# Performance work log

Measured on AMD Instinct MI355X. Metric: run time of the kernel, lower is better.

The kernel has to match this reference:

```python
import jax, jax.numpy as jnp
import numpy as np

D_MODEL = 1024
NUM_HEADS = 16
HEAD_DIM = D_MODEL // NUM_HEADS


def setup_inputs() -> dict:
    key = jax.random.key(0)
    ks = jax.random.split(key, 11)
    B, S = 4, 2048
    s = 1.0 / np.sqrt(D_MODEL)
    inp = {
        "query": jax.random.normal(ks[0], (B, S, D_MODEL), jnp.float32),
        "key": jax.random.normal(ks[1], (B, S, D_MODEL), jnp.float32),
        "value": jax.random.normal(ks[2], (B, S, D_MODEL), jnp.float32),
        "Wq": jax.random.normal(ks[3], (D_MODEL, D_MODEL), jnp.float32) * s,
        "bq": jnp.zeros((D_MODEL,), jnp.float32),
        "Wk": jax.random.normal(ks[4], (D_MODEL, D_MODEL), jnp.float32) * s,
        "bk": jnp.zeros((D_MODEL,), jnp.float32),
        "Wv": jax.random.normal(ks[5], (D_MODEL, D_MODEL), jnp.float32) * s,
        "bv": jnp.zeros((D_MODEL,), jnp.float32),
        "Wo": jax.random.normal(ks[6], (D_MODEL, D_MODEL), jnp.float32) * s,
        "bo": jnp.zeros((D_MODEL,), jnp.float32),
    }
    return inp


def reference(query, key, value, Wq, bq, Wk, bk, Wv, bv, Wo, bo):
    B, S, _ = query.shape
    def proj(x, W, b):  # [B,S,D] -> [B,H,S,hd]
        y = jnp.einsum("bsd,ed->bse", x, W) + b
        return y.reshape(B, -1, NUM_HEADS, HEAD_DIM).transpose(0, 2, 1, 3)
    q = proj(query, Wq, bq)
    k = proj(key, Wk, bk)
    v = proj(value, Wv, bv)
    scores = jnp.einsum("bhqd,bhkd->bhqk", q, k) / np.sqrt(HEAD_DIM).astype(jnp.float32)
    attn = jax.nn.softmax(scores, axis=-1)
    out = jnp.einsum("bhqk,bhkd->bhqd", attn, v)
    out = out.transpose(0, 2, 1, 3).reshape(B, -1, D_MODEL)
    return jnp.einsum("bsd,ed->bse", out, Wo) + bo
```

## Files before the change

### kernel.cpp

```cpp
#include <hip/hip_runtime.h>
#include <math.h>

#define DM    1024
#define NH    16
#define HD    64
#define SEQ   2048
#define BATCH 4
#define TOKENS (BATCH * SEQ)

typedef _Float16 half2v __attribute__((ext_vector_type(2)));
typedef __fp16   fp16x2 __attribute__((ext_vector_type(2)));
typedef _Float16 half4  __attribute__((ext_vector_type(4)));
typedef _Float16 half8  __attribute__((ext_vector_type(8)));
typedef float    f32x4  __attribute__((ext_vector_type(4)));
typedef float    f32x16 __attribute__((ext_vector_type(16)));
typedef unsigned int u32x2 __attribute__((ext_vector_type(2)));
typedef unsigned int u32x4 __attribute__((ext_vector_type(4)));

typedef const __attribute__((address_space(1))) void* gas_p;
typedef __attribute__((address_space(3))) void*       las_p;

__device__ __forceinline__ void gload_lds16(const void* g, void* l) {
    __builtin_amdgcn_global_load_lds((gas_p)g, (las_p)l, 16, 0, 0);
}

__device__ __forceinline__ unsigned pack2u(float a, float b) {
    fp16x2 r = __builtin_amdgcn_cvt_pkrtz(a, b);
    return __builtin_bit_cast(unsigned, r);
}

#define MFMA16(a, b, c) __builtin_amdgcn_mfma_f32_16x16x32_f16((a), (b), (c), 0, 0, 0)
#define MFMA32(a, b, c) __builtin_amdgcn_mfma_f32_32x32x16_f16((a), (b), (c), 0, 0, 0)

__global__ __launch_bounds__(256) void cvt_all(
    const float* __restrict__ q, const float* __restrict__ k,
    const float* __restrict__ v, const float* __restrict__ wq,
    const float* __restrict__ wk, const float* __restrict__ wv,
    const float* __restrict__ wo, _Float16* __restrict__ dst)
{
    const size_t TD = (size_t)TOKENS * DM, WD = (size_t)DM * DM;
    const size_t i = ((size_t)blockIdx.x * 256 + threadIdx.x) * 4;
    const float* s; size_t off;
    if      (i <     TD)          { s = q;  off = i; }
    else if (i < 2 * TD)          { s = k;  off = i - TD; }
    else if (i < 3 * TD)          { s = v;  off = i - 2 * TD; }
    else if (i < 3 * TD + WD)     { s = wq; off = i - 3 * TD; }
    else if (i < 3 * TD + 2 * WD) { s = wk; off = i - 3 * TD - WD; }
    else if (i < 3 * TD + 3 * WD) { s = wv; off = i - 3 * TD - 2 * WD; }
    else                          { s = wo; off = i - 3 * TD - 3 * WD; }
    const float4 x = *(const float4*)(s + off);
    half4 h = { (_Float16)x.x, (_Float16)x.y, (_Float16)x.z, (_Float16)x.w };
    *(half4*)(dst + i) = h;
}

__global__ __launch_bounds__(256) void qkv_gemm(
    const _Float16* __restrict__ Abase, const _Float16* __restrict__ Wbase,
    const float* __restrict__ bq, const float* __restrict__ bk,
    const float* __restrict__ bv, _Float16* __restrict__ Cbase, float qscale)
{
    __shared__ __align__(16) _Float16 As[128 * 32];
    __shared__ __align__(16) _Float16 Ws[128 * 32];

    const int z = blockIdx.z;
    const size_t TD = (size_t)TOKENS * DM, WD = (size_t)DM * DM;
    const _Float16* A = Abase + (size_t)z * TD;
    const _Float16* W = Wbase + (size_t)z * WD;
    const float* bias = (z == 0) ? bq : (z == 1) ? bk : bv;
    _Float16* C = Cbase + (size_t)z * TD;
    const float scale = (z == 0) ? qscale : 1.0f;

    const int t = threadIdx.x;
    const int w = t >> 6, l = t & 63;
    const int tx = l & 15, quad = l >> 4;
    const int m0 = blockIdx.x * 128, n0 = blockIdx.y * 128;
    const int wm = (w & 1) * 64, wn = (w >> 1) * 64;
    const int srow = t >> 2, schk = t & 3;

    const _Float16* Ag = A + (size_t)m0 * DM;
    const _Float16* Wg = W + (size_t)n0 * DM;

    f32x4 acc[4][4] = {};

    for (int k0 = 0; k0 < DM; k0 += 32) {
        __syncthreads();
        #pragma unroll
        for (int i = 0; i < 2; ++i) {
            gload_lds16(Ag + (size_t)(i * 64 + srow) * DM + k0 + schk * 8,
                        As + (size_t)(i * 256 + (t & ~63)) * 8);
            gload_lds16(Wg + (size_t)(i * 64 + srow) * DM + k0 + schk * 8,
                        Ws + (size_t)(i * 256 + (t & ~63)) * 8);
        }
        __syncthreads();

        half8 af[4], bf[4];
        #pragma unroll
        for (int mt = 0; mt < 4; ++mt)
            af[mt] = *(const half8*)(As + (wm + mt * 16 + tx) * 32 + quad * 8);
        #pragma unroll
        for (int nt = 0; nt < 4; ++nt)
            bf[nt] = *(const half8*)(Ws + (wn + nt * 16 + tx) * 32 + quad * 8);
        #pragma unroll
        for (int mt = 0; mt < 4; ++mt)
            #pragma unroll
            for (int nt = 0; nt < 4; ++nt)
                acc[mt][nt] = MFMA16(af[mt], bf[nt], acc[mt][nt]);
    }

    float bsv[4];
    #pragma unroll
    for (int nt = 0; nt < 4; ++nt) bsv[nt] = bias[n0 + wn + nt * 16 + tx];

    #pragma unroll
    for (int mt = 0; mt < 4; ++mt) {
        #pragma unroll
        for (int nt = 0; nt < 4; ++nt) {
            const int n = n0 + wn + nt * 16 + tx;
            const int mr0 = m0 + wm + mt * 16 + quad * 4;
            const int h = n >> 6, d = n & 63;
            if (z < 2) {
                #pragma unroll
                for (int r = 0; r < 4; ++r) {
                    const int m = mr0 + r;
                    const int b = m >> 11, s = m & (SEQ - 1);
                    const float vv = (acc[mt][nt][r] + bsv[nt]) * scale;
                    C[(((size_t)b * NH + h) * SEQ + s) * HD + d] = (_Float16)vv;
                }
            } else {
                const int b = mr0 >> 11, s0 = mr0 & (SEQ - 1);
                half4 hv = { (_Float16)(acc[mt][nt][0] + bsv[nt]),
                             (_Float16)(acc[mt][nt][1] + bsv[nt]),
                             (_Float16)(acc[mt][nt][2] + bsv[nt]),
                             (_Float16)(acc[mt][nt][3] + bsv[nt]) };
                *(half4*)(C + (((size_t)b * NH + h) * HD + d) * SEQ + s0) = hv;
            }
        }
    }
}

__global__ __launch_bounds__(256) void out_gemm(
    const _Float16* __restrict__ A, const _Float16* __restrict__ W,
    const float* __restrict__ bias, float* __restrict__ C)
{
    __shared__ __align__(16) _Float16 As[128 * 32];
    __shared__ __align__(16) _Float16 Ws[128 * 32];

    const int t = threadIdx.x;
    const int w = t >> 6, l = t & 63;
    const int tx = l & 15, quad = l >> 4;
    const int m0 = blockIdx.x * 128, n0 = blockIdx.y * 128;
    const int wm = (w & 1) * 64, wn = (w >> 1) * 64;
    const int srow = t >> 2, schk = t & 3;

    const _Float16* Ag = A + (size_t)m0 * DM;
    const _Float16* Wg = W + (size_t)n0 * DM;

    f32x4 acc[4][4] = {};

    for (int k0 = 0; k0 < DM; k0 += 32) {
        __syncthreads();
        #pragma unroll
        for (int i = 0; i < 2; ++i) {
            gload_lds16(Ag + (size_t)(i * 64 + srow) * DM + k0 + schk * 8,
                        As + (size_t)(i * 256 + (t & ~63)) * 8);
            gload_lds16(Wg + (size_t)(i * 64 + srow) * DM + k0 + schk * 8,
                        Ws + (size_t)(i * 256 + (t & ~63)) * 8);
        }
        __syncthreads();

        half8 af[4], bf[4];
        #pragma unroll
        for (int mt = 0; mt < 4; ++mt)
            af[mt] = *(const half8*)(As + (wm + mt * 16 + tx) * 32 + quad * 8);
        #pragma unroll
        for (int nt = 0; nt < 4; ++nt)
            bf[nt] = *(const half8*)(Ws + (wn + nt * 16 + tx) * 32 + quad * 8);
        #pragma unroll
        for (int mt = 0; mt < 4; ++mt)
            #pragma unroll
            for (int nt = 0; nt < 4; ++nt)
                acc[mt][nt] = MFMA16(af[mt], bf[nt], acc[mt][nt]);
    }

    float bsv[4];
    #pragma unroll
    for (int nt = 0; nt < 4; ++nt) bsv[nt] = bias[n0 + wn + nt * 16 + tx];

    #pragma unroll
    for (int mt = 0; mt < 4; ++mt)
        #pragma unroll
        for (int nt = 0; nt < 4; ++nt) {
            const int n = n0 + wn + nt * 16 + tx;
            const int mr0 = m0 + wm + mt * 16 + quad * 4;
            #pragma unroll
            for (int r = 0; r < 4; ++r)
                C[(size_t)(mr0 + r) * DM + n] = acc[mt][nt][r] + bsv[nt];
        }
}

__global__ __launch_bounds__(256, 3) void flash16(
    const _Float16* __restrict__ Q, const _Float16* __restrict__ K,
    const _Float16* __restrict__ Vt, _Float16* __restrict__ AO)
{
    __shared__ __align__(16) char pool[34816];
    __shared__ float lW[128];

    const int t = threadIdx.x, w = t >> 6, l = t & 63;
    const int lid = l & 31, hl = l >> 5;

    const int bid = blockIdx.x;
    const int xcd = bid & 7, loc = bid >> 3;
    const int bh = xcd * 8 + (loc >> 4);
    const int q0 = (loc & 15) * 128;
    const int b = bh >> 4, h = bh & 15;

    const _Float16* Qg = Q + ((size_t)bh * SEQ + q0 + w * 32) * HD;
    const _Float16* Kg = K + (size_t)bh * SEQ * HD;
    const _Float16* Vg = Vt + (size_t)bh * HD * SEQ;

    const int srow = l >> 3;
    const int schk = (l & 7) ^ srow;

    half8 Qf[4];
    #pragma unroll
    for (int ks = 0; ks < 4; ++ks)
        Qf[ks] = *(const half8*)(Qg + (size_t)lid * HD + ks * 16 + hl * 8);

    f32x16 Oa[2] = {};
    float l2 = 0.f;
    const half2v one2 = { (_Float16)1.0f, (_Float16)1.0f };

    {
        _Float16* KL = (_Float16*)(pool);
        _Float16* VL = (_Float16*)(pool + 16384);
        #pragma unroll
        for (int jj = 0; jj < 2; ++jj) {
            const int j = w + jj * 4;
            const int row = 8 * j + srow;
            gload_lds16(Kg + (size_t)row * HD + schk * 8, KL + j * 512);
            gload_lds16(Vg + (size_t)row * SEQ + schk * 8, VL + j * 512);
        }
    }

    for (int it = 0; it < SEQ / 64; ++it) {
        __syncthreads();

        if (it < SEQ / 64 - 1) {
            const int kb = (it + 1) * 64;
            _Float16* KL = (_Float16*)(pool + ((it + 1) & 1) * 8192);
            _Float16* VL = (_Float16*)(pool + 16384 + ((it + 1) & 1) * 8192);
            #pragma unroll
            for (int jj = 0; jj < 2; ++jj) {
                const int j = w + jj * 4;
                const int row = 8 * j + srow;
                gload_lds16(Kg + (size_t)(kb + row) * HD + schk * 8, KL + j * 512);
                gload_lds16(Vg + (size_t)row * SEQ + kb + schk * 8, VL + j * 512);
            }
        }

        const _Float16* KL = (const _Float16*)(pool + (it & 1) * 8192);
        const _Float16* VL = (const _Float16*)(pool + 16384 + (it & 1) * 8192);

        half8 kf[2][4];
        #pragma unroll
        for (int kt = 0; kt < 2; ++kt)
            #pragma unroll
            for (int ks = 0; ks < 4; ++ks)
                kf[kt][ks] = *(const half8*)(KL + (kt * 32 + lid) * 64 +
                                             (((ks * 2 + hl) ^ (lid & 7)) * 8));

        f32x16 sacc[2];
        __builtin_amdgcn_s_setprio(1);
        #pragma unroll
        for (int kt = 0; kt < 2; ++kt) {
            f32x16 s = {};
            #pragma unroll
            for (int ks = 0; ks < 4; ++ks)
                s = MFMA32(kf[kt][ks], Qf[ks], s);
            sacc[kt] = s;
        }
        __builtin_amdgcn_s_setprio(0);

        half8 vf[4][2];
        #pragma unroll
        for (int kstep = 0; kstep < 4; ++kstep)
            #pragma unroll
            for (int dt = 0; dt < 2; ++dt)
                vf[kstep][dt] = *(const half8*)(VL + (dt * 32 + lid) * 64 +
                                                (((kstep * 2 + hl) ^ (lid & 7)) * 8));

        unsigned cf[2][4][2];
        #pragma unroll
        for (int kt = 0; kt < 2; ++kt)
            #pragma unroll
            for (int g = 0; g < 4; ++g) {
                const float p0 = __builtin_amdgcn_exp2f(sacc[kt][g * 4 + 0]);
                const float p1 = __builtin_amdgcn_exp2f(sacc[kt][g * 4 + 1]);
                const float p2 = __builtin_amdgcn_exp2f(sacc[kt][g * 4 + 2]);
                const float p3 = __builtin_amdgcn_exp2f(sacc[kt][g * 4 + 3]);
                const unsigned ca = pack2u(p0, p1);
                const unsigned cb = pack2u(p2, p3);
                l2 = __builtin_amdgcn_fdot2(__builtin_bit_cast(half2v, ca), one2, l2, false);
                l2 = __builtin_amdgcn_fdot2(__builtin_bit_cast(half2v, cb), one2, l2, false);
                cf[kt][g][0] = ca;
                cf[kt][g][1] = cb;
            }

        __builtin_amdgcn_s_setprio(1);
        #pragma unroll
        for (int kstep = 0; kstep < 4; ++kstep) {
            const int kt = kstep >> 1, g0 = (kstep & 1) * 2;
            const u32x2 r0 = __builtin_amdgcn_permlane32_swap(
                cf[kt][g0][0], cf[kt][g0 + 1][0], false, false);
            const u32x2 r1 = __builtin_amdgcn_permlane32_swap(
                cf[kt][g0][1], cf[kt][g0 + 1][1], false, false);
            const u32x4 pw = { r0[0], r1[0], r0[1], r1[1] };
            const half8 pa = __builtin_bit_cast(half8, pw);
            #pragma unroll
            for (int dt = 0; dt < 2; ++dt)
                Oa[dt] = MFMA32(pa, vf[kstep][dt], Oa[dt]);
        }
        __builtin_amdgcn_s_setprio(0);
    }

    l2 += __shfl_xor(l2, 32, 64);
    if (l < 32) lW[w * 32 + l] = l2;
    __syncthreads();

    float* Ob = (float*)pool;
    #pragma unroll
    for (int dt = 0; dt < 2; ++dt)
        #pragma unroll
        for (int g = 0; g < 4; ++g)
            #pragma unroll
            for (int r = 0; r < 4; ++r)
                Ob[(w * 32 + g * 8 + hl * 4 + r) * 68 + dt * 32 + lid] = Oa[dt][g * 4 + r];
    __syncthreads();

    {
        const int row = t >> 1, cb = (t & 1) * 32;
        const float inv = 1.0f / lW[row];
        _Float16* dst = AO + ((size_t)b * SEQ + q0 + row) * DM + h * HD + cb;
        #pragma unroll
        for (int j = 0; j < 32; j += 8) {
            const f32x4 o0 = *(const f32x4*)(Ob + row * 68 + cb + j);
            const f32x4 o1 = *(const f32x4*)(Ob + row * 68 + cb + j + 4);
            half8 hv = { (_Float16)(o0[0] * inv), (_Float16)(o0[1] * inv),
                         (_Float16)(o0[2] * inv), (_Float16)(o0[3] * inv),
                         (_Float16)(o1[0] * inv), (_Float16)(o1[1] * inv),
                         (_Float16)(o1[2] * inv), (_Float16)(o1[3] * inv) };
            *(half8*)(dst + j) = hv;
        }
    }
}

extern "C" void kernel_launch(void* const* d_in, const int* in_sizes, int n_in,
                              void* d_out, int out_size, void* d_ws, size_t ws_size,
                              hipStream_t stream)
{
    const float* q  = (const float*)d_in[0];
    const float* k  = (const float*)d_in[1];
    const float* v  = (const float*)d_in[2];
    const float* Wq = (const float*)d_in[3];
    const float* bq = (const float*)d_in[4];
    const float* Wk = (const float*)d_in[5];
    const float* bk = (const float*)d_in[6];
    const float* Wv = (const float*)d_in[7];
    const float* bv = (const float*)d_in[8];
    const float* Wo = (const float*)d_in[9];
    const float* bo = (const float*)d_in[10];
    float* out = (float*)d_out;

    const size_t TD = (size_t)TOKENS * DM;
    const size_t WD = (size_t)DM * DM;
    _Float16* ws = (_Float16*)d_ws;
    _Float16* cvtbase = ws;
    _Float16* q16  = ws;
    _Float16* wq16 = ws + 3 * TD;
    _Float16* wo16 = wq16 + 3 * WD;
    _Float16* Qw   = ws + 3 * TD + 4 * WD;
    _Float16* Kw   = Qw + TD;
    _Float16* Vtw  = Kw + TD;
    _Float16* AOw  = Vtw + TD;

    const int gC = (int)((3 * TD + 4 * WD) / 4 / 256);
    cvt_all<<<gC, 256, 0, stream>>>(q, k, v, Wq, Wk, Wv, Wo, cvtbase);

    const float qscale = 0.18033688011112042f;
    qkv_gemm<<<dim3(TOKENS / 128, DM / 128, 3), 256, 0, stream>>>(
        q16, wq16, bq, bk, bv, Qw, qscale);

    flash16<<<dim3((SEQ / 128) * BATCH * NH), 256, 0, stream>>>(Qw, Kw, Vtw, AOw);

    out_gemm<<<dim3(TOKENS / 128, DM / 128, 1), 256, 0, stream>>>(AOw, wo16, bo, out);
}
```

Baseline: 340.4 us.

## Process 64 query rows per wave in flash attention with 128-thread blocks

```diff
diff --git a/kernel.cpp b/kernel.cpp
--- a/kernel.cpp
+++ b/kernel.cpp
@@ -197,7 +197,7 @@
         }
 }
 
-__global__ __launch_bounds__(256, 3) void flash16(
+__global__ __launch_bounds__(128, 2) void flash16(
     const _Float16* __restrict__ Q, const _Float16* __restrict__ K,
     const _Float16* __restrict__ Vt, _Float16* __restrict__ AO)
 {
@@ -213,28 +213,30 @@
     const int q0 = (loc & 15) * 128;
     const int b = bh >> 4, h = bh & 15;
 
-    const _Float16* Qg = Q + ((size_t)bh * SEQ + q0 + w * 32) * HD;
+    const _Float16* Qg = Q + ((size_t)bh * SEQ + q0 + w * 64) * HD;
     const _Float16* Kg = K + (size_t)bh * SEQ * HD;
     const _Float16* Vg = Vt + (size_t)bh * HD * SEQ;
 
     const int srow = l >> 3;
     const int schk = (l & 7) ^ srow;
 
-    half8 Qf[4];
-    #pragma unroll
-    for (int ks = 0; ks < 4; ++ks)
-        Qf[ks] = *(const half8*)(Qg + (size_t)lid * HD + ks * 16 + hl * 8);
-
-    f32x16 Oa[2] = {};
-    float l2 = 0.f;
+    half8 Qf[2][4];
+    #pragma unroll
+    for (int qq = 0; qq < 2; ++qq)
+        #pragma unroll
+        for (int ks = 0; ks < 4; ++ks)
+            Qf[qq][ks] = *(const half8*)(Qg + (size_t)(qq * 32 + lid) * HD + ks * 16 + hl * 8);
+
+    f32x16 Oa[2][2] = {};
+    float l2[2] = {0.f, 0.f};
     const half2v one2 = { (_Float16)1.0f, (_Float16)1.0f };
 
     {
         _Float16* KL = (_Float16*)(pool);
         _Float16* VL = (_Float16*)(pool + 16384);
         #pragma unroll
-        for (int jj = 0; jj < 2; ++jj) {
-            const int j = w + jj * 4;
+        for (int jj = 0; jj < 4; ++jj) {
+            const int j = w + jj * 2;
             const int row = 8 * j + srow;
             gload_lds16(Kg + (size_t)row * HD + schk * 8, KL + j * 512);
             gload_lds16(Vg + (size_t)row * SEQ + schk * 8, VL + j * 512);
@@ -249,8 +251,8 @@
             _Float16* KL = (_Float16*)(pool + ((it + 1) & 1) * 8192);
             _Float16* VL = (_Float16*)(pool + 16384 + ((it + 1) & 1) * 8192);
             #pragma unroll
-            for (int jj = 0; jj < 2; ++jj) {
-                const int j = w + jj * 4;
+            for (int jj = 0; jj < 4; ++jj) {
+                const int j = w + jj * 2;
                 const int row = 8 * j + srow;
                 gload_lds16(Kg + (size_t)(kb + row) * HD + schk * 8, KL + j * 512);
                 gload_lds16(Vg + (size_t)row * SEQ + kb + schk * 8, VL + j * 512);
@@ -268,17 +270,49 @@
                 kf[kt][ks] = *(const half8*)(KL + (kt * 32 + lid) * 64 +
                                              (((ks * 2 + hl) ^ (lid & 7)) * 8));
 
-        f32x16 sacc[2];
-        __builtin_amdgcn_s_setprio(1);
-        #pragma unroll
-        for (int kt = 0; kt < 2; ++kt) {
-            f32x16 s = {};
-            #pragma unroll
-            for (int ks = 0; ks < 4; ++ks)
-                s = MFMA32(kf[kt][ks], Qf[ks], s);
-            sacc[kt] = s;
-        }
-        __builtin_amdgcn_s_setprio(0);
+        half8 pa[2][4];
+        #pragma unroll
+        for (int qq = 0; qq < 2; ++qq) {
+            f32x16 sacc[2];
+            __builtin_amdgcn_s_setprio(1);
+            #pragma unroll
+            for (int kt = 0; kt < 2; ++kt) {
+                f32x16 s = {};
+                #pragma unroll
+                for (int ks = 0; ks < 4; ++ks)
+                    s = MFMA32(kf[kt][ks], Qf[qq][ks], s);
+                sacc[kt] = s;
+            }
+            __builtin_amdgcn_s_setprio(0);
+
+            unsigned cf[2][4][2];
+            #pragma unroll
+            for (int kt = 0; kt < 2; ++kt)
+                #pragma unroll
+                for (int g = 0; g < 4; ++g) {
+                    const float p0 = __builtin_amdgcn_exp2f(sacc[kt][g * 4 + 0]);
+                    const float p1 = __builtin_amdgcn_exp2f(sacc[kt][g * 4 + 1]);
+                    const float p2 = __builtin_amdgcn_exp2f(sacc[kt][g * 4 + 2]);
+                    const float p3 = __builtin_amdgcn_exp2f(sacc[kt][g * 4 + 3]);
+                    const unsigned ca = pack2u(p0, p1);
+                    const unsigned cb = pack2u(p2, p3);
+                    l2[qq] = __builtin_amdgcn_fdot2(__builtin_bit_cast(half2v, ca), one2, l2[qq], false);
+                    l2[qq] = __builtin_amdgcn_fdot2(__builtin_bit_cast(half2v, cb), one2, l2[qq], false);
+                    cf[kt][g][0] = ca;
+                    cf[kt][g][1] = cb;
+                }
+
+            #pragma unroll
+            for (int kstep = 0; kstep < 4; ++kstep) {
+                const int kt = kstep >> 1, g0 = (kstep & 1) * 2;
+                const u32x2 r0 = __builtin_amdgcn_permlane32_swap(
+                    cf[kt][g0][0], cf[kt][g0 + 1][0], false, false);
+                const u32x2 r1 = __builtin_amdgcn_permlane32_swap(
+                    cf[kt][g0][1], cf[kt][g0 + 1][1], false, false);
+                const u32x4 pw = { r0[0], r1[0], r0[1], r1[1] };
+                pa[qq][kstep] = __builtin_bit_cast(half8, pw);
+            }
+        }
 
         half8 vf[4][2];
         #pragma unroll
@@ -288,62 +322,47 @@
                 vf[kstep][dt] = *(const half8*)(VL + (dt * 32 + lid) * 64 +
                                                 (((kstep * 2 + hl) ^ (lid & 7)) * 8));
 
-        unsigned cf[2][4][2];
-        #pragma unroll
-        for (int kt = 0; kt < 2; ++kt)
-            #pragma unroll
-            for (int g = 0; g < 4; ++g) {
-                const float p0 = __builtin_amdgcn_exp2f(sacc[kt][g * 4 + 0]);
-                const float p1 = __builtin_amdgcn_exp2f(sacc[kt][g * 4 + 1]);
-                const float p2 = __builtin_amdgcn_exp2f(sacc[kt][g * 4 + 2]);
-                const float p3 = __builtin_amdgcn_exp2f(sacc[kt][g * 4 + 3]);
-                const unsigned ca = pack2u(p0, p1);
-                const unsigned cb = pack2u(p2, p3);
-                l2 = __builtin_amdgcn_fdot2(__builtin_bit_cast(half2v, ca), one2, l2, false);
-                l2 = __builtin_amdgcn_fdot2(__builtin_bit_cast(half2v, cb), one2, l2, false);
-                cf[kt][g][0] = ca;
-                cf[kt][g][1] = cb;
-            }
-
         __builtin_amdgcn_s_setprio(1);
         #pragma unroll
-        for (int kstep = 0; kstep < 4; ++kstep) {
-            const int kt = kstep >> 1, g0 = (kstep & 1) * 2;
-            const u32x2 r0 = __builtin_amdgcn_permlane32_swap(
-                cf[kt][g0][0], cf[kt][g0 + 1][0], false, false);
-            const u32x2 r1 = __builtin_amdgcn_permlane32_swap(
-                cf[kt][g0][1], cf[kt][g0 + 1][1], false, false);
-            const u32x4 pw = { r0[0], r1[0], r0[1], r1[1] };
-            const half8 pa = __builtin_bit_cast(half8, pw);
-            #pragma unroll
-            for (int dt = 0; dt < 2; ++dt)
-                Oa[dt] = MFMA32(pa, vf[kstep][dt], Oa[dt]);
-        }
+        for (int kstep = 0; kstep < 4; ++kstep)
+            #pragma unroll
+            for (int qq = 0; qq < 2; ++qq)
+                #pragma unroll
+                for (int dt = 0; dt < 2; ++dt)
+                    Oa[qq][dt] = MFMA32(pa[qq][kstep], vf[kstep][dt], Oa[qq][dt]);
         __builtin_amdgcn_s_setprio(0);
     }
 
-    l2 += __shfl_xor(l2, 32, 64);
-    if (l < 32) lW[w * 32 + l] = l2;
+    #pragma unroll
+    for (int qq = 0; qq < 2; ++qq)
+        l2[qq] += __shfl_xor(l2[qq], 32, 64);
+    if (l < 32) {
+        lW[w * 64 + l] = l2[0];
+        lW[w * 64 + 32 + l] = l2[1];
+    }
     __syncthreads();
 
     float* Ob = (float*)pool;
     #pragma unroll
-    for (int dt = 0; dt < 2; ++dt)
-        #pragma unroll
-        for (int g = 0; g < 4; ++g)
-            #pragma unroll
-            for (int r = 0; r < 4; ++r)
-                Ob[(w * 32 + g * 8 + hl * 4 + r) * 68 + dt * 32 + lid] = Oa[dt][g * 4 + r];
+    for (int qq = 0; qq < 2; ++qq)
+        #pragma unroll
+        for (int dt = 0; dt < 2; ++dt)
+            #pragma unroll
+            for (int g = 0; g < 4; ++g)
+                #pragma unroll
+                for (int r = 0; r < 4; ++r)
+                    Ob[(w * 64 + qq * 32 + g * 8 + hl * 4 + r) * 68 + dt * 32 + lid] =
+                        Oa[qq][dt][g * 4 + r];
     __syncthreads();
 
     {
-        const int row = t >> 1, cb = (t & 1) * 32;
+        const int row = t;
         const float inv = 1.0f / lW[row];
-        _Float16* dst = AO + ((size_t)b * SEQ + q0 + row) * DM + h * HD + cb;
-        #pragma unroll
-        for (int j = 0; j < 32; j += 8) {
-            const f32x4 o0 = *(const f32x4*)(Ob + row * 68 + cb + j);
-            const f32x4 o1 = *(const f32x4*)(Ob + row * 68 + cb + j + 4);
+        _Float16* dst = AO + ((size_t)b * SEQ + q0 + row) * DM + h * HD;
+        #pragma unroll
+        for (int j = 0; j < 64; j += 8) {
+            const f32x4 o0 = *(const f32x4*)(Ob + row * 68 + j);
+            const f32x4 o1 = *(const f32x4*)(Ob + row * 68 + j + 4);
             half8 hv = { (_Float16)(o0[0] * inv), (_Float16)(o0[1] * inv),
                          (_Float16)(o0[2] * inv), (_Float16)(o0[3] * inv),
                          (_Float16)(o1[0] * inv), (_Float16)(o1[1] * inv),
@@ -389,7 +408,7 @@
     qkv_gemm<<<dim3(TOKENS / 128, DM / 128, 3), 256, 0, stream>>>(
         q16, wq16, bq, bk, bv, Qw, qscale);
 
-    flash16<<<dim3((SEQ / 128) * BATCH * NH), 256, 0, stream>>>(Qw, Kw, Vtw, AOw);
+    flash16<<<dim3((SEQ / 128) * BATCH * NH), 128, 0, stream>>>(Qw, Kw, Vtw, AOw);
 
     out_gemm<<<dim3(TOKENS / 128, DM / 128, 1), 256, 0, stream>>>(AOw, wo16, bo, out);
 }
```

Measured after the change: 344.6 us. Within noise of the previous version (+1.2%).

## Double-buffer LDS tiles and XOR-swizzle chunks in projection GEMMs

Applied to the files above, without the earlier changes.

```diff
diff --git a/kernel.cpp b/kernel.cpp
--- a/kernel.cpp
+++ b/kernel.cpp
@@ -58,8 +58,8 @@
     const float* __restrict__ bq, const float* __restrict__ bk,
     const float* __restrict__ bv, _Float16* __restrict__ Cbase, float qscale)
 {
-    __shared__ __align__(16) _Float16 As[128 * 32];
-    __shared__ __align__(16) _Float16 Ws[128 * 32];
+    __shared__ __align__(16) _Float16 As[2][128 * 32];
+    __shared__ __align__(16) _Float16 Ws[2][128 * 32];
 
     const int z = blockIdx.z;
     const size_t TD = (size_t)TOKENS * DM, WD = (size_t)DM * DM;
@@ -74,31 +74,46 @@
     const int tx = l & 15, quad = l >> 4;
     const int m0 = blockIdx.x * 128, n0 = blockIdx.y * 128;
     const int wm = (w & 1) * 64, wn = (w >> 1) * 64;
-    const int srow = t >> 2, schk = t & 3;
+    const int srow = t >> 2;
+    const int schk = (t & 3) ^ (srow & 3);
 
     const _Float16* Ag = A + (size_t)m0 * DM;
     const _Float16* Wg = W + (size_t)n0 * DM;
 
     f32x4 acc[4][4] = {};
 
+    #pragma unroll
+    for (int i = 0; i < 2; ++i) {
+        gload_lds16(Ag + (size_t)(i * 64 + srow) * DM + schk * 8,
+                    As[0] + (size_t)(i * 256 + (t & ~63)) * 8);
+        gload_lds16(Wg + (size_t)(i * 64 + srow) * DM + schk * 8,
+                    Ws[0] + (size_t)(i * 256 + (t & ~63)) * 8);
+    }
+
     for (int k0 = 0; k0 < DM; k0 += 32) {
         __syncthreads();
-        #pragma unroll
-        for (int i = 0; i < 2; ++i) {
-            gload_lds16(Ag + (size_t)(i * 64 + srow) * DM + k0 + schk * 8,
-                        As + (size_t)(i * 256 + (t & ~63)) * 8);
-            gload_lds16(Wg + (size_t)(i * 64 + srow) * DM + k0 + schk * 8,
-                        Ws + (size_t)(i * 256 + (t & ~63)) * 8);
-        }
-        __syncthreads();
+        const int cur = (k0 >> 5) & 1;
+        if (k0 + 32 < DM) {
+            #pragma unroll
+            for (int i = 0; i < 2; ++i) {
+                gload_lds16(Ag + (size_t)(i * 64 + srow) * DM + k0 + 32 + schk * 8,
+                            As[cur ^ 1] + (size_t)(i * 256 + (t & ~63)) * 8);
+                gload_lds16(Wg + (size_t)(i * 64 + srow) * DM + k0 + 32 + schk * 8,
+                            Ws[cur ^ 1] + (size_t)(i * 256 + (t & ~63)) * 8);
+            }
+        }
 
         half8 af[4], bf[4];
         #pragma unroll
-        for (int mt = 0; mt < 4; ++mt)
-            af[mt] = *(const half8*)(As + (wm + mt * 16 + tx) * 32 + quad * 8);
-        #pragma unroll
-        for (int nt = 0; nt < 4; ++nt)
-            bf[nt] = *(const half8*)(Ws + (wn + nt * 16 + tx) * 32 + quad * 8);
+        for (int mt = 0; mt < 4; ++mt) {
+            const int r = wm + mt * 16 + tx;
+            af[mt] = *(const half8*)(As[cur] + r * 32 + ((quad ^ (r & 3)) * 8));
+        }
+        #pragma unroll
+        for (int nt = 0; nt < 4; ++nt) {
+            const int r = wn + nt * 16 + tx;
+            bf[nt] = *(const half8*)(Ws[cur] + r * 32 + ((quad ^ (r & 3)) * 8));
+        }
         #pragma unroll
         for (int mt = 0; mt < 4; ++mt)
             #pragma unroll
@@ -141,39 +156,54 @@
     const _Float16* __restrict__ A, const _Float16* __restrict__ W,
     const float* __restrict__ bias, float* __restrict__ C)
 {
-    __shared__ __align__(16) _Float16 As[128 * 32];
-    __shared__ __align__(16) _Float16 Ws[128 * 32];
+    __shared__ __align__(16) _Float16 As[2][128 * 32];
+    __shared__ __align__(16) _Float16 Ws[2][128 * 32];
 
     const int t = threadIdx.x;
     const int w = t >> 6, l = t & 63;
     const int tx = l & 15, quad = l >> 4;
     const int m0 = blockIdx.x * 128, n0 = blockIdx.y * 128;
     const int wm = (w & 1) * 64, wn = (w >> 1) * 64;
-    const int srow = t >> 2, schk = t & 3;
+    const int srow = t >> 2;
+    const int schk = (t & 3) ^ (srow & 3);
 
     const _Float16* Ag = A + (size_t)m0 * DM;
     const _Float16* Wg = W + (size_t)n0 * DM;
 
     f32x4 acc[4][4] = {};
 
+    #pragma unroll
+    for (int i = 0; i < 2; ++i) {
+        gload_lds16(Ag + (size_t)(i * 64 + srow) * DM + schk * 8,
+                    As[0] + (size_t)(i * 256 + (t & ~63)) * 8);
+        gload_lds16(Wg + (size_t)(i * 64 + srow) * DM + schk * 8,
+                    Ws[0] + (size_t)(i * 256 + (t & ~63)) * 8);
+    }
+
     for (int k0 = 0; k0 < DM; k0 += 32) {
         __syncthreads();
-        #pragma unroll
-        for (int i = 0; i < 2; ++i) {
-            gload_lds16(Ag + (size_t)(i * 64 + srow) * DM + k0 + schk * 8,
-                        As + (size_t)(i * 256 + (t & ~63)) * 8);
-            gload_lds16(Wg + (size_t)(i * 64 + srow) * DM + k0 + schk * 8,
-                        Ws + (size_t)(i * 256 + (t & ~63)) * 8);
-        }
-        __syncthreads();
+        const int cur = (k0 >> 5) & 1;
+        if (k0 + 32 < DM) {
+            #pragma unroll
+            for (int i = 0; i < 2; ++i) {
+                gload_lds16(Ag + (size_t)(i * 64 + srow) * DM + k0 + 32 + schk * 8,
+                            As[cur ^ 1] + (size_t)(i * 256 + (t & ~63)) * 8);
+                gload_lds16(Wg + (size_t)(i * 64 + srow) * DM + k0 + 32 + schk * 8,
+                            Ws[cur ^ 1] + (size_t)(i * 256 + (t & ~63)) * 8);
+            }
+        }
 
         half8 af[4], bf[4];
         #pragma unroll
-        for (int mt = 0; mt < 4; ++mt)
-            af[mt] = *(const half8*)(As + (wm + mt * 16 + tx) * 32 + quad * 8);
-        #pragma unroll
-        for (int nt = 0; nt < 4; ++nt)
-            bf[nt] = *(const half8*)(Ws + (wn + nt * 16 + tx) * 32 + quad * 8);
+        for (int mt = 0; mt < 4; ++mt) {
+            const int r = wm + mt * 16 + tx;
+            af[mt] = *(const half8*)(As[cur] + r * 32 + ((quad ^ (r & 3)) * 8));
+        }
+        #pragma unroll
+        for (int nt = 0; nt < 4; ++nt) {
+            const int r = wn + nt * 16 + tx;
+            bf[nt] = *(const half8*)(Ws[cur] + r * 32 + ((quad ^ (r & 3)) * 8));
+        }
         #pragma unroll
         for (int mt = 0; mt < 4; ++mt)
             #pragma unroll
```

New measurement: 346.0 us. Within noise of the previous version (+1.6%).
